# Kernel tuning notes

Hardware: AMD Instinct MI355X
Metric: run time of the kernel (lower is better)

Reference implementation:

```python
import jax, jax.numpy as jnp
import numpy as np

N, L, D = 100000, 4, 64          # nodes, gcn layers, emb_dim
B, S = 16384, 32                 # links, intersection-set size
INP, RELD, NREL, NDIST = 32, 32, 200, 11
PSD = L * D                      # param_set_dim = 256


def setup_inputs() -> dict:
    key = jax.random.key(0)
    ks = jax.random.split(key, 16)
    return {
        "node_repr": jax.random.normal(ks[0], (N, L, D), jnp.float32),
        "node_feat": jax.random.normal(ks[1], (N, INP), jnp.float32),
        "head_idx": jax.random.randint(ks[2], (B,), 0, N, jnp.int32),
        "rel_idx": jax.random.randint(ks[3], (B,), 0, NREL, jnp.int32),
        "tail_idx": jax.random.randint(ks[4], (B,), 0, N, jnp.int32),
        "dist": jax.random.randint(ks[5], (B,), 0, NDIST, jnp.int32),
        "inter_count": jax.random.randint(ks[6], (B, S), 0, N, jnp.int32),
        "rel_emb": jax.random.normal(ks[7], (NREL, RELD), jnp.float32),
        "dist_emb": jax.random.normal(ks[8], (NDIST, D), jnp.float32),
        "head_W": jax.random.normal(ks[9], (PSD + D, INP), jnp.float32) * 0.05,
        "head_b": jnp.zeros((INP,), jnp.float32),
        "tail_W": jax.random.normal(ks[10], (PSD + D, INP), jnp.float32) * 0.05,
        "tail_b": jnp.zeros((INP,), jnp.float32),
        "W1": jax.random.normal(ks[11], (2 * PSD + RELD + 2 * INP + PSD, 64), jnp.float32) * 0.05,
        "b1": jnp.zeros((64,), jnp.float32),
        "W2": jax.random.normal(ks[12], (64, 32), jnp.float32) * 0.05,
        "b2": jnp.zeros((32,), jnp.float32),
        "W3": jax.random.normal(ks[13], (32, 1), jnp.float32) * 0.05,
        "b3": jnp.zeros((1,), jnp.float32),
    }


def reference(node_repr, node_feat, head_idx, rel_idx, tail_idx, dist, inter_count,
              rel_emb, dist_emb, head_W, head_b, tail_W, tail_b,
              W1, b1, W2, b2, W3, b3):
    flat = node_repr.reshape(node_repr.shape[0], -1)           # [N, PSD]
    head_repr = flat[head_idx]                                 # [B, PSD]
    tail_repr = flat[tail_idx]                                 # [B, PSD]
    rel_repr = rel_emb[rel_idx]                                # [B, RELD]

    # masked gather + mean over the intersection set (-1 entries masked out)
    sign = jnp.sign(inter_count + 1).astype(flat.dtype)        # [B, S]
    mid = flat[jnp.abs(inter_count)] * sign[:, :, None]        # [B, S, PSD]
    mid = mid.sum(axis=1)                                      # [B, PSD]
    cnt = jnp.clip(jnp.sum(inter_count != -1, axis=1), 1, None)
    mid_repr = mid / cnt[:, None].astype(flat.dtype)

    dist_repr = dist_emb[dist]                                 # [B, D]

    md = jnp.concatenate([mid_repr, dist_repr], axis=1)        # [B, PSD+D]
    head_pred = md @ head_W + head_b                           # [B, INP]
    tail_pred = md @ tail_W + tail_b
    head_init_feat = node_feat[head_idx]
    tail_init_feat = node_feat[tail_idx]

    g_rep = jnp.concatenate(
        [head_repr, tail_repr, rel_repr, mid_repr, head_init_feat, tail_init_feat], axis=1)
    h = jax.nn.relu(g_rep @ W1 + b1)
    h = jax.nn.relu(h @ W2 + b2)
    output = h @ W3 + b3                                       # [B, 1]
    return (output, head_pred, tail_pred, head_init_feat, tail_init_feat)
```

## Files before the change

### kernel.cpp

```cpp
#include <hip/hip_runtime.h>
#include <cstddef>
#include <cstdint>

typedef __bf16 bf16x8 __attribute__((ext_vector_type(8)));
typedef float  f32x4  __attribute__((ext_vector_type(4)));

#define NLINK 8
#define X_STRIDE 936
#define H1_STRIDE 66
#define WTC_ELEMS (128 * 928)
#define WTC_BYTES (WTC_ELEMS * 2)
#define SHADOW_OFF 262144

__device__ __forceinline__ float b2f(unsigned short u) {
    unsigned int x = (unsigned int)u << 16;
    return __builtin_bit_cast(float, x);
}
__device__ __forceinline__ unsigned short f2b(float f) {
    unsigned int u = __builtin_bit_cast(unsigned int, f);
    u += 0x7FFFu + ((u >> 16) & 1u);
    return (unsigned short)(u >> 16);
}

__global__ void prep_weights(const float* __restrict__ W1,
                             const float* __restrict__ headW,
                             const float* __restrict__ tailW,
                             unsigned short* __restrict__ WTc) {
    const int n = blockIdx.x;
    for (int k = threadIdx.x; k < 928; k += blockDim.x) {
        float v = 0.f;
        if (n < 64) {
            if (k < 864) v = W1[(size_t)k * 64 + n];
        } else {
            const int c = (n < 96) ? (n - 64) : (n - 96);
            const float* W = (n < 96) ? headW : tailW;
            if (k >= 544 && k < 800)      v = W[(size_t)(k - 544) * 32 + c];
            else if (k >= 864 && k < 928) v = W[(size_t)(256 + (k - 864)) * 32 + c];
        }
        WTc[(size_t)n * 928 + k] = f2b(v);
    }
}

__global__ __launch_bounds__(256) void conv_table(const float* __restrict__ src,
                                                  unsigned short* __restrict__ dst,
                                                  long n4) {
    const long stride = (long)gridDim.x * blockDim.x;
    for (long i = (long)blockIdx.x * blockDim.x + threadIdx.x; i < n4; i += stride) {
        float4 v = ((const float4*)src)[i];
        ushort4 o;
        o.x = f2b(v.x); o.y = f2b(v.y); o.z = f2b(v.z); o.w = f2b(v.w);
        ((ushort4*)dst)[i] = o;
    }
}

__device__ __forceinline__ bf16x8 gather_Bfrag(const float* __restrict__ W1,
                                               const float* __restrict__ hW,
                                               const float* __restrict__ tW,
                                               int n, int k0) {
    unsigned short r[8];
    if (n < 64) {
        #pragma unroll
        for (int j = 0; j < 8; ++j) {
            const int k = k0 + j;
            r[j] = (k < 864) ? f2b(W1[(size_t)k * 64 + n]) : (unsigned short)0;
        }
    } else {
        const float* W = (n < 96) ? hW : tW;
        const int c = (n < 96) ? (n - 64) : (n - 96);
        #pragma unroll
        for (int j = 0; j < 8; ++j) {
            const int k = k0 + j;
            float v = 0.f;
            if (k >= 544 && k < 800)      v = W[(size_t)(k - 544) * 32 + c];
            else if (k >= 864 && k < 928) v = W[(size_t)(256 + (k - 864)) * 32 + c];
            r[j] = f2b(v);
        }
    }
    unsigned short tmp[8];
    #pragma unroll
    for (int j = 0; j < 8; ++j) tmp[j] = r[j];
    return __builtin_bit_cast(bf16x8, *(const uint4*)tmp);
}

template <int MODE>
__global__ __launch_bounds__(256, 4) void fused_main(
    const float* __restrict__ node_repr,
    const float* __restrict__ node_feat,
    const int* __restrict__ head_idx,
    const int* __restrict__ rel_idx,
    const int* __restrict__ tail_idx,
    const int* __restrict__ dist,
    const int* __restrict__ inter,
    const float* __restrict__ rel_emb,
    const float* __restrict__ dist_emb,
    const float* __restrict__ b1p,
    const float* __restrict__ head_bp,
    const float* __restrict__ tail_bp,
    const float* __restrict__ W2p,
    const float* __restrict__ b2p,
    const float* __restrict__ W3p,
    const float* __restrict__ b3p,
    const unsigned short* __restrict__ WTc,
    const unsigned short* __restrict__ shadow,
    const float* __restrict__ W1p,
    const float* __restrict__ headWp,
    const float* __restrict__ tailWp,
    float* __restrict__ out,
    int B)
{
    extern __shared__ char smem[];
    unsigned short* sX  = (unsigned short*)smem;
    unsigned short* sH1 = (unsigned short*)(smem + NLINK * X_STRIDE * 2);

    const int tid  = threadIdx.x;
    const int w    = tid >> 6;
    const int lane = tid & 63;
    const int g0   = blockIdx.x * NLINK;

    float* out0   = out;
    float* out_hp = out + B;
    float* out_tp = out + B + (size_t)B * 32;
    float* out_hf = out + B + (size_t)B * 64;
    float* out_tf = out + B + (size_t)B * 96;

    for (int li = 0; li < 2; ++li) {
        const int L = w * 2 + li;
        const int g = g0 + L;
        if (g >= B) continue;

        const int hidx = head_idx[g];
        const int tidx = tail_idx[g];
        const int ridx = rel_idx[g];
        const int didx = dist[g];
        const int c4 = lane * 4;
        const int* icp = inter + (size_t)g * 32;

        float a0 = 0.f, a1 = 0.f, a2 = 0.f, a3 = 0.f;
        int cnt = 0;

        if (MODE == 2) {
            ushort4 hb = *(const ushort4*)(shadow + (size_t)hidx * 256 + c4);
            ushort4 tb = *(const ushort4*)(shadow + (size_t)tidx * 256 + c4);
            *(ushort4*)(sX + (size_t)L * X_STRIDE + c4)       = hb;
            *(ushort4*)(sX + (size_t)L * X_STRIDE + 256 + c4) = tb;

            #pragma unroll
            for (int s = 0; s < 32; ++s) {
                const int ic = icp[s];
                const int idx = (ic >= 0) ? ic : -ic;
                const float sg = (ic == -1) ? 0.f : ((ic >= 0) ? 1.f : -1.f);
                ushort4 v = *(const ushort4*)(shadow + (size_t)idx * 256 + c4);
                a0 += sg * b2f(v.x); a1 += sg * b2f(v.y);
                a2 += sg * b2f(v.z); a3 += sg * b2f(v.w);
                cnt += (ic != -1) ? 1 : 0;
            }
        } else {
            float4 hr = *(const float4*)(node_repr + (size_t)hidx * 256 + c4);
            float4 tr = *(const float4*)(node_repr + (size_t)tidx * 256 + c4);
            ushort4 hb; hb.x = f2b(hr.x); hb.y = f2b(hr.y); hb.z = f2b(hr.z); hb.w = f2b(hr.w);
            ushort4 tb; tb.x = f2b(tr.x); tb.y = f2b(tr.y); tb.z = f2b(tr.z); tb.w = f2b(tr.w);
            *(ushort4*)(sX + (size_t)L * X_STRIDE + c4)       = hb;
            *(ushort4*)(sX + (size_t)L * X_STRIDE + 256 + c4) = tb;

            #pragma unroll
            for (int s = 0; s < 32; ++s) {
                const int ic = icp[s];
                const int idx = (ic >= 0) ? ic : -ic;
                const float sg = (ic == -1) ? 0.f : ((ic >= 0) ? 1.f : -1.f);
                float4 v = *(const float4*)(node_repr + (size_t)idx * 256 + c4);
                a0 += sg * v.x; a1 += sg * v.y;
                a2 += sg * v.z; a3 += sg * v.w;
                cnt += (ic != -1) ? 1 : 0;
            }
        }

        const float inv = 1.0f / (float)(cnt > 0 ? cnt : 1);
        ushort4 mv;
        mv.x = f2b(a0 * inv); mv.y = f2b(a1 * inv);
        mv.z = f2b(a2 * inv); mv.w = f2b(a3 * inv);
        *(ushort4*)(sX + (size_t)L * X_STRIDE + 544 + c4) = mv;

        if (lane < 32) {
            const float hf = node_feat[(size_t)hidx * 32 + lane];
            const float tf = node_feat[(size_t)tidx * 32 + lane];
            const float rv = rel_emb[(size_t)ridx * 32 + lane];
            sX[(size_t)L * X_STRIDE + 800 + lane] = f2b(hf);
            sX[(size_t)L * X_STRIDE + 832 + lane] = f2b(tf);
            sX[(size_t)L * X_STRIDE + 512 + lane] = f2b(rv);
            out_hf[(size_t)g * 32 + lane] = hf;
            out_tf[(size_t)g * 32 + lane] = tf;
        }
        sX[(size_t)L * X_STRIDE + 864 + lane] = f2b(dist_emb[(size_t)didx * 64 + lane]);
    }
    __syncthreads();

    const int col16 = lane & 15;
    const int row8  = lane & 7;
    const int quad  = lane >> 4;
    const int n0    = w * 32;

    f32x4 accv[2] = {{0.f,0.f,0.f,0.f},{0.f,0.f,0.f,0.f}};

    const unsigned short* aP = sX + (size_t)row8 * X_STRIDE + quad * 8;

    if (MODE >= 1) {
        const unsigned short* bP0 = WTc + (size_t)(n0 +  0 + col16) * 928 + quad * 8;
        const unsigned short* bP1 = WTc + (size_t)(n0 + 16 + col16) * 928 + quad * 8;
        for (int ks = 0; ks < 29; ++ks) {
            const bf16x8 af = __builtin_bit_cast(bf16x8, *(const uint4*)(aP + ks * 32));
            bf16x8 b0 = __builtin_bit_cast(bf16x8, *(const uint4*)(bP0 + ks * 32));
            bf16x8 b1 = __builtin_bit_cast(bf16x8, *(const uint4*)(bP1 + ks * 32));
            accv[0] = __builtin_amdgcn_mfma_f32_16x16x32_bf16(af, b0, accv[0], 0, 0, 0);
            accv[1] = __builtin_amdgcn_mfma_f32_16x16x32_bf16(af, b1, accv[1], 0, 0, 0);
        }
    } else {
        for (int ks = 0; ks < 29; ++ks) {
            const int k0 = ks * 32 + quad * 8;
            const bf16x8 af = __builtin_bit_cast(bf16x8, *(const uint4*)(aP + ks * 32));
            bf16x8 b0 = gather_Bfrag(W1p, headWp, tailWp, n0 +  0 + col16, k0);
            bf16x8 b1 = gather_Bfrag(W1p, headWp, tailWp, n0 + 16 + col16, k0);
            accv[0] = __builtin_amdgcn_mfma_f32_16x16x32_bf16(af, b0, accv[0], 0, 0, 0);
            accv[1] = __builtin_amdgcn_mfma_f32_16x16x32_bf16(af, b1, accv[1], 0, 0, 0);
        }
    }

    if (n0 < 64) {
        #pragma unroll
        for (int t = 0; t < 2; ++t) {
            const int n = n0 + t * 16 + col16;
            const float bias = b1p[n];
            #pragma unroll
            for (int r = 0; r < 4; ++r) {
                const int row = quad * 4 + r;
                if (row < NLINK) {
                    float v = accv[t][r] + bias;
                    v = v > 0.f ? v : 0.f;
                    sH1[(size_t)row * H1_STRIDE + n] = f2b(v);
                }
            }
        }
    } else {
        const bool isH = (n0 < 96);
        const float* bp = isH ? head_bp : tail_bp;
        float* dst = isH ? out_hp : out_tp;
        #pragma unroll
        for (int t = 0; t < 2; ++t) {
            const int c = (n0 - (isH ? 64 : 96)) + t * 16 + col16;
            const float bias = bp[c];
            #pragma unroll
            for (int r = 0; r < 4; ++r) {
                const int row = quad * 4 + r;
                const int m = g0 + row;
                if (row < NLINK && m < B) dst[(size_t)m * 32 + c] = accv[t][r] + bias;
            }
        }
    }
    __syncthreads();

    const int half = lane >> 5;
    const int c    = lane & 31;
    const float w3v = W3p[c];
    const float b2v = b2p[c];
    const float b3v = b3p[0];
    {
        const int L = w * 2 + half;
        float acc = 0.f;
        #pragma unroll 8
        for (int k = 0; k < 64; ++k)
            acc += b2f(sH1[(size_t)L * H1_STRIDE + k]) * W2p[(size_t)k * 32 + c];
        const float h2 = fmaxf(acc + b2v, 0.f);
        float p = h2 * w3v;
        p += __shfl_xor(p, 16);
        p += __shfl_xor(p, 8);
        p += __shfl_xor(p, 4);
        p += __shfl_xor(p, 2);
        p += __shfl_xor(p, 1);
        if (c == 0 && (g0 + L) < B) out0[g0 + L] = p + b3v;
    }
}

extern "C" void kernel_launch(void* const* d_in, const int* in_sizes, int n_in,
                              void* d_out, int out_size, void* d_ws, size_t ws_size,
                              hipStream_t stream) {
    const float* node_repr = (const float*)d_in[0];
    const float* node_feat = (const float*)d_in[1];
    const int* head_idx = (const int*)d_in[2];
    const int* rel_idx  = (const int*)d_in[3];
    const int* tail_idx = (const int*)d_in[4];
    const int* dist     = (const int*)d_in[5];
    const int* inter    = (const int*)d_in[6];
    const float* rel_emb  = (const float*)d_in[7];
    const float* dist_emb = (const float*)d_in[8];
    const float* head_W   = (const float*)d_in[9];
    const float* head_b   = (const float*)d_in[10];
    const float* tail_W   = (const float*)d_in[11];
    const float* tail_b   = (const float*)d_in[12];
    const float* W1       = (const float*)d_in[13];
    const float* b1       = (const float*)d_in[14];
    const float* W2       = (const float*)d_in[15];
    const float* b2       = (const float*)d_in[16];
    const float* W3       = (const float*)d_in[17];
    const float* b3       = (const float*)d_in[18];

    const int B = in_sizes[2];
    const long nrepr = in_sizes[0];
    float* out = (float*)d_out;

    const int grid = (B + NLINK - 1) / NLINK;
    const size_t lds = (size_t)NLINK * X_STRIDE * 2 + (size_t)NLINK * H1_STRIDE * 2;

    const size_t shadow_bytes = (size_t)nrepr * 2;
    const size_t need2 = (size_t)SHADOW_OFF + shadow_bytes;

    if (ws_size >= need2) {
        unsigned short* WTc    = (unsigned short*)d_ws;
        unsigned short* shadow = (unsigned short*)((char*)d_ws + SHADOW_OFF);
        hipLaunchKernelGGL(prep_weights, dim3(128), dim3(256), 0, stream,
                           W1, head_W, tail_W, WTc);
        hipLaunchKernelGGL(conv_table, dim3(2048), dim3(256), 0, stream,
                           node_repr, shadow, nrepr / 4);
        hipLaunchKernelGGL((fused_main<2>), dim3(grid), dim3(256), lds, stream,
                           node_repr, node_feat, head_idx, rel_idx, tail_idx, dist, inter,
                           rel_emb, dist_emb, b1, head_b, tail_b, W2, b2, W3, b3,
                           WTc, shadow, W1, head_W, tail_W, out, B);
    } else if (ws_size >= (size_t)WTC_BYTES) {
        unsigned short* WTc = (unsigned short*)d_ws;
        hipLaunchKernelGGL(prep_weights, dim3(128), dim3(256), 0, stream,
                           W1, head_W, tail_W, WTc);
        hipLaunchKernelGGL((fused_main<1>), dim3(grid), dim3(256), lds, stream,
                           node_repr, node_feat, head_idx, rel_idx, tail_idx, dist, inter,
                           rel_emb, dist_emb, b1, head_b, tail_b, W2, b2, W3, b3,
                           WTc, (const unsigned short*)nullptr, W1, head_W, tail_W, out, B);
    } else {
        hipLaunchKernelGGL((fused_main<0>), dim3(grid), dim3(256), lds, stream,
                           node_repr, node_feat, head_idx, rel_idx, tail_idx, dist, inter,
                           rel_emb, dist_emb, b1, head_b, tail_b, W2, b2, W3, b3,
                           (const unsigned short*)nullptr, (const unsigned short*)nullptr,
                           W1, head_W, tail_W, out, B);
    }
}
```

Baseline: 273.5 us.

## Stage intersection-row gathers through LDS with async global_load_lds

In the bf16 shadow path, head, tail and intersection-set row gathers now go through global_load_lds straight into a per-wave LDS staging buffer, 16 rows at a time, and are read back for the signed sum. The goal is to put many gathers in flight with fewer VGPRs and no register round-trip. The cost is an extra 32KB of LDS per block, so launch bounds drop to 3 blocks per CU. The conversion kernel grid is also doubled. The 4-byte lane layout in the async copies has to match the ushort4 readback indexing.

```diff
diff --git a/kernel.cpp b/kernel.cpp
--- a/kernel.cpp
+++ b/kernel.cpp
@@ -11,6 +11,16 @@
 #define WTC_ELEMS (128 * 928)
 #define WTC_BYTES (WTC_ELEMS * 2)
 #define SHADOW_OFF 262144
+#define STAGE_ROWS 16
+#define STAGE_US_PER_WAVE (STAGE_ROWS * 256)
+
+#define GLD4(gsrc, ldst)                                                              \
+    __builtin_amdgcn_global_load_lds(                                                 \
+        (const __attribute__((address_space(1))) unsigned int*)(gsrc),                \
+        (__attribute__((address_space(3))) unsigned int*)(ldst), 4, 0, 0)
+
+#define WAIT_VM0()   __builtin_amdgcn_s_waitcnt(0x0F70)
+#define WAIT_LGKM0() __builtin_amdgcn_s_waitcnt(0xC07F)
 
 __device__ __forceinline__ float b2f(unsigned short u) {
     unsigned int x = (unsigned int)u << 16;
@@ -83,7 +93,7 @@
 }
 
 template <int MODE>
-__global__ __launch_bounds__(256, 4) void fused_main(
+__global__ __launch_bounds__(256, 3) void fused_main(
     const float* __restrict__ node_repr,
     const float* __restrict__ node_feat,
     const int* __restrict__ head_idx,
@@ -111,6 +121,8 @@
     extern __shared__ char smem[];
     unsigned short* sX  = (unsigned short*)smem;
     unsigned short* sH1 = (unsigned short*)(smem + NLINK * X_STRIDE * 2);
+    unsigned short* sStage = (unsigned short*)(smem + NLINK * X_STRIDE * 2
+                                                    + NLINK * H1_STRIDE * 2);
 
     const int tid  = threadIdx.x;
     const int w    = tid >> 6;
@@ -139,20 +151,37 @@
         int cnt = 0;
 
         if (MODE == 2) {
-            ushort4 hb = *(const ushort4*)(shadow + (size_t)hidx * 256 + c4);
-            ushort4 tb = *(const ushort4*)(shadow + (size_t)tidx * 256 + c4);
-            *(ushort4*)(sX + (size_t)L * X_STRIDE + c4)       = hb;
-            *(ushort4*)(sX + (size_t)L * X_STRIDE + 256 + c4) = tb;
-
+            {
+                const unsigned short* hrow = shadow + (size_t)hidx * 256 + lane * 2;
+                const unsigned short* trow = shadow + (size_t)tidx * 256 + lane * 2;
+                unsigned short* dh = sX + (size_t)L * X_STRIDE;
+                unsigned short* dt = sX + (size_t)L * X_STRIDE + 256;
+                GLD4(hrow, dh); GLD4(hrow + 128, dh + 128);
+                GLD4(trow, dt); GLD4(trow + 128, dt + 128);
+            }
+            unsigned short* stW = sStage + (size_t)w * STAGE_US_PER_WAVE;
             #pragma unroll
-            for (int s = 0; s < 32; ++s) {
-                const int ic = icp[s];
-                const int idx = (ic >= 0) ? ic : -ic;
-                const float sg = (ic == -1) ? 0.f : ((ic >= 0) ? 1.f : -1.f);
-                ushort4 v = *(const ushort4*)(shadow + (size_t)idx * 256 + c4);
-                a0 += sg * b2f(v.x); a1 += sg * b2f(v.y);
-                a2 += sg * b2f(v.z); a3 += sg * b2f(v.w);
-                cnt += (ic != -1) ? 1 : 0;
+            for (int half = 0; half < 2; ++half) {
+                const int sb = half * STAGE_ROWS;
+                #pragma unroll
+                for (int s = 0; s < STAGE_ROWS; ++s) {
+                    const int ic  = icp[sb + s];
+                    const int idx = (ic >= 0) ? ic : -ic;
+                    const unsigned short* row = shadow + (size_t)idx * 256 + lane * 2;
+                    unsigned short* dstls = stW + s * 256;
+                    GLD4(row, dstls); GLD4(row + 128, dstls + 128);
+                }
+                WAIT_VM0();
+                #pragma unroll
+                for (int s = 0; s < STAGE_ROWS; ++s) {
+                    const int ic = icp[sb + s];
+                    const float sg = (ic == -1) ? 0.f : ((ic >= 0) ? 1.f : -1.f);
+                    cnt += (ic != -1) ? 1 : 0;
+                    ushort4 v = *(const ushort4*)(stW + s * 256 + lane * 4);
+                    a0 += sg * b2f(v.x); a1 += sg * b2f(v.y);
+                    a2 += sg * b2f(v.z); a3 += sg * b2f(v.w);
+                }
+                WAIT_LGKM0();
             }
         } else {
             float4 hr = *(const float4*)(node_repr + (size_t)hidx * 256 + c4);
@@ -307,7 +336,8 @@
     float* out = (float*)d_out;
 
     const int grid = (B + NLINK - 1) / NLINK;
-    const size_t lds = (size_t)NLINK * X_STRIDE * 2 + (size_t)NLINK * H1_STRIDE * 2;
+    const size_t lds = (size_t)NLINK * X_STRIDE * 2 + (size_t)NLINK * H1_STRIDE * 2
+                     + (size_t)4 * STAGE_US_PER_WAVE * 2;
 
     const size_t shadow_bytes = (size_t)nrepr * 2;
     const size_t need2 = (size_t)SHADOW_OFF + shadow_bytes;
@@ -317,7 +347,7 @@
         unsigned short* shadow = (unsigned short*)((char*)d_ws + SHADOW_OFF);
         hipLaunchKernelGGL(prep_weights, dim3(128), dim3(256), 0, stream,
                            W1, head_W, tail_W, WTc);
-        hipLaunchKernelGGL(conv_table, dim3(2048), dim3(256), 0, stream,
+        hipLaunchKernelGGL(conv_table, dim3(4096), dim3(256), 0, stream,
                            node_repr, shadow, nrepr / 4);
         hipLaunchKernelGGL((fused_main<2>), dim3(grid), dim3(256), lds, stream,
                            node_repr, node_feat, head_idx, rel_idx, tail_idx, dist, inter,
```

New measurement: 286.4 us. 4.7% more time.
